# Optimization experiments

Measured on AMD Instinct MI355X. Metric: run time of the kernel, lower is better.

## Reference

```python
import jax, jax.numpy as jnp
import numpy as np

T, B, D_IN, H = 512, 128, 1024, 2048

def _lstm_cell(x, h, c, W_ih, W_hh, b):
    # PyTorch LSTMCell gate order: i, f, g, o
    gates = x @ W_ih.T + h @ W_hh.T + b  # [B, 4H]
    i, f, g, o = jnp.split(gates, 4, axis=-1)
    c_new = jax.nn.sigmoid(f) * c + jax.nn.sigmoid(i) * jnp.tanh(g)
    h_new = jax.nn.sigmoid(o) * jnp.tanh(c_new)
    return h_new, c_new

def setup_inputs() -> dict:
    key = jax.random.key(0)
    ks = jax.random.split(key, 12)
    k = 1.0 / np.sqrt(H)  # torch LSTMCell init range
    u = lambda kk, shape: jax.random.uniform(kk, shape, jnp.float32, -k, k)
    return {
        "input_seq": jax.random.normal(ks[0], (T, B, D_IN), jnp.float32),
        "h0": jax.random.normal(ks[1], (2, B, H), jnp.float32),
        "c0": jax.random.normal(ks[2], (2, B, H), jnp.float32),
        "W_ih0": u(ks[3], (4 * H, D_IN)),
        "W_hh0": u(ks[4], (4 * H, H)),
        "b0": u(ks[5], (4 * H,)),
        "W_ih1": u(ks[6], (4 * H, H)),
        "W_hh1": u(ks[7], (4 * H, H)),
        "b1": u(ks[8], (4 * H,)),
    }

def reference(input_seq, h0, c0, W_ih0, W_hh0, b0, W_ih1, W_hh1, b1):
    def step(carry, x_t):
        h0_, c0_, h1_, c1_ = carry
        h0n, c0n = _lstm_cell(x_t, h0_, c0_, W_ih0, W_hh0, b0)
        h1n, c1n = _lstm_cell(h0n, h1_, c1_, W_ih1, W_hh1, b1)
        return (h0n, c0n, h1n, c1n), None

    init = (h0[0], c0[0], h0[1], c0[1])
    (h0f, c0f, h1f, c1f), _ = jax.lax.scan(step, init, input_seq)
    return h1f  # last layer hidden at final timestep [B, H]
```

## Files before the change

### kernel.cpp

```cpp
#include <hip/hip_runtime.h>
#include <stdint.h>
#include <stddef.h>

#define T_STEPS 512
#define B_SZ    128
#define DIN     1024
#define H_SZ    2048
#define NG      8192
#define BH      (B_SZ * H_SZ)

typedef __attribute__((ext_vector_type(8))) short bf16x8;
typedef __attribute__((ext_vector_type(16))) float f32x16;

static __device__ __forceinline__ unsigned short f2bf(float x) {
  unsigned int u = __float_as_uint(x);
  u += 0x7fffu + ((u >> 16) & 1u);
  return (unsigned short)(u >> 16);
}

static __device__ __forceinline__ float sigm(float x) {
  return 1.0f / (1.0f + __expf(-x));
}
static __device__ __forceinline__ float tanh_(float x) {
  float e = __expf(-2.0f * fabsf(x));
  float t = (1.0f - e) / (1.0f + e);
  return x < 0.0f ? -t : t;
}

static __device__ __forceinline__ void async_load16(const void* gsrc, void* ldst) {
  __builtin_amdgcn_global_load_lds(
      (__attribute__((address_space(1))) void*)(const_cast<void*>(gsrc)),
      (__attribute__((address_space(3))) void*)ldst,
      16, 0, 0);
}

static __device__ __forceinline__ void wg_barrier_pinned() {
  __builtin_amdgcn_s_barrier();
  asm volatile("" ::: "memory");
  __builtin_amdgcn_sched_barrier(0);
}

static __device__ __forceinline__ void publish(unsigned* flag, unsigned epoch) {
  __syncthreads();
  if (threadIdx.x == 0) {
    __threadfence();
    __hip_atomic_store(flag, epoch, __ATOMIC_RELEASE, __HIP_MEMORY_SCOPE_AGENT);
  }
}
static __device__ __forceinline__ void await(const unsigned* flag, unsigned epoch) {
  if (threadIdx.x == 0)
    while (__hip_atomic_load(flag, __ATOMIC_ACQUIRE, __HIP_MEMORY_SCOPE_AGENT) < epoch)
      __builtin_amdgcn_s_sleep(8);
  __syncthreads();
}

__global__ void cvt_x_bf16(const float4* __restrict__ in, ushort4* __restrict__ out, int n4) {
  int i = blockIdx.x * blockDim.x + threadIdx.x;
  int st = gridDim.x * blockDim.x;
  for (; i < n4; i += st) {
    float4 v = in[i];
    ushort4 o;
    o.x = f2bf(v.x); o.y = f2bf(v.y); o.z = f2bf(v.z); o.w = f2bf(v.w);
    out[i] = o;
  }
}

__global__ void build_wcat(const float* __restrict__ wa, const float* __restrict__ wb,
                           unsigned short* __restrict__ outw, int ka, int K) {
  int k = blockIdx.x * blockDim.x + threadIdx.x;
  int n = blockIdx.y;
  if (k >= K) return;
  int kb = K - ka;
  float v = (k < ka) ? wa[(size_t)n * ka + k]
                     : wb[(size_t)n * kb + (k - ka)];
  outw[(size_t)n * K + k] = f2bf(v);
}

__global__ void init_state(const float* __restrict__ h0, const float* __restrict__ c0,
                           unsigned short* __restrict__ hb0, unsigned short* __restrict__ hb1,
                           float* __restrict__ cws, unsigned* __restrict__ flags) {
  int i = blockIdx.x * blockDim.x + threadIdx.x;
  if (i < 256) flags[i] = 0u;
  if (i < BH) {
    hb0[i] = f2bf(h0[i]);
    hb1[i] = f2bf(h0[BH + i]);
    cws[i] = c0[i];
    cws[BH + i] = c0[BH + i];
  }
}

template<int KT>
static __device__ __forceinline__ void gemm_ks(
    unsigned short (*Bbuf)[128 * 64],
    const unsigned short* __restrict__ a0, int s0, int ksplit,
    const unsigned short* __restrict__ a1,
    int kofs,
    const unsigned short* __restrict__ w, int wstr,
    int tid, int lane, int wv, int n0h,
    f32x16 (&acc)[4])
{
  const int arow = wv * 32 + (lane & 31);
  const unsigned short* r0p = a0 + (size_t)arow * s0;
  const unsigned short* r1p = a1 + (size_t)arow * H_SZ;
  const int khi = (lane >> 5) << 3;

  auto loadA = [&](int kt, bf16x8 (&A)[4]) {
    const int kbg = kofs + (kt << 6);
    const bool sA = kbg < ksplit;
    const unsigned short* bp = (sA ? r0p + kbg : r1p + (kbg - ksplit)) + khi;
#pragma unroll
    for (int cc = 0; cc < 4; ++cc)
      A[cc] = *(const bf16x8*)(bp + cc * 16);
  };

  auto stageB = [&](int kt) {
    const int kbg = kofs + (kt << 6);
#pragma unroll
    for (int it = 0; it < 4; ++it) {
      int cid = it * 256 + tid;
      int nl  = cid >> 3;
      int chs = (cid & 7) ^ (nl & 7);
      int nn  = ((nl >> 5) << 11) + n0h + (nl & 31);
      const unsigned short* src = w + (size_t)nn * wstr + kbg + (chs << 3);
      async_load16(src, &Bbuf[kt & 3][(it * 256 + wv * 64) * 8]);
    }
  };

  auto iter = [&](int kt, bf16x8 (&A)[4]) {
    if (kt + 3 < KT) stageB(kt + 3);
    const int bq = kt & 3;
#pragma unroll
    for (int cc = 0; cc < 4; ++cc) {
      const int chunk = (((cc << 1) + (lane >> 5)) ^ (lane & 7)) << 3;
      bf16x8 bfr[4];
#pragma unroll
      for (int ct = 0; ct < 4; ++ct)
        bfr[ct] = *(const bf16x8*)&Bbuf[bq][(ct * 32 + (lane & 31)) * 64 + chunk];
#pragma unroll
      for (int ct = 0; ct < 4; ++ct)
        acc[ct] = __builtin_amdgcn_mfma_f32_32x32x16_bf16(A[cc], bfr[ct], acc[ct], 0, 0, 0);
    }
    if (kt + 4 < KT) loadA(kt + 4, A);
    int rem = KT - 1 - kt;
    if (rem >= 4)      asm volatile("s_waitcnt vmcnt(20)" ::: "memory");
    else if (rem == 3) asm volatile("s_waitcnt vmcnt(16)" ::: "memory");
    else if (rem == 2) asm volatile("s_waitcnt vmcnt(8)"  ::: "memory");
    else if (rem == 1) asm volatile("s_waitcnt vmcnt(0)"  ::: "memory");
    if (rem > 0) wg_barrier_pinned();
  };

  asm volatile("s_waitcnt vmcnt(0)" ::: "memory");

  bf16x8 A0[4], A1[4], A2[4], A3[4];
  stageB(0); loadA(0, A0);
  stageB(1); loadA(1, A1);
  stageB(2); loadA(2, A2);
  loadA(3, A3);
  asm volatile("s_waitcnt vmcnt(24)" ::: "memory");
  wg_barrier_pinned();

  for (int kt = 0; kt < KT; kt += 4) {
    iter(kt,     A0);
    iter(kt + 1, A1);
    iter(kt + 2, A2);
    iter(kt + 3, A3);
  }
}

static __device__ __forceinline__ void store_partial(
    const f32x16 (&acc)[4], float* __restrict__ p, int lane, int wv) {
  const int col = lane & 31;
  const int rbase = wv * 32 + ((lane >> 5) << 2);
#pragma unroll
  for (int ct = 0; ct < 4; ++ct)
#pragma unroll
    for (int reg = 0; reg < 16; ++reg) {
      int row = rbase + (reg & 3) + ((reg >> 2) << 3);
      p[((ct << 7) + row) * 32 + col] = acc[ct][reg];
    }
}
static __device__ __forceinline__ void combine_add(
    f32x16 (&acc)[4], const float* __restrict__ p, int lane, int wv) {
  const int col = lane & 31;
  const int rbase = wv * 32 + ((lane >> 5) << 2);
#pragma unroll
  for (int ct = 0; ct < 4; ++ct)
#pragma unroll
    for (int reg = 0; reg < 16; ++reg) {
      int row = rbase + (reg & 3) + ((reg >> 2) << 3);
      acc[ct][reg] += p[((ct << 7) + row) * 32 + col];
    }
}

static __device__ __forceinline__ void lstm_epilogue(
    const f32x16 (&acc)[4], const float* __restrict__ bias,
    float* __restrict__ c, unsigned short* __restrict__ hout,
    float* __restrict__ fout, int lane, int wv, int n0h) {
  const int hc = n0h + (lane & 31);
  const float bi  = bias[hc];
  const float bff = bias[H_SZ + hc];
  const float bg  = bias[2 * H_SZ + hc];
  const float bo  = bias[3 * H_SZ + hc];
  const int rbase = wv * 32 + ((lane >> 5) << 2);
#pragma unroll
  for (int reg = 0; reg < 16; ++reg) {
    int row = rbase + (reg & 3) + ((reg >> 2) << 3);
    size_t idx = (size_t)row * H_SZ + hc;
    float iv = sigm(acc[0][reg] + bi);
    float fv = sigm(acc[1][reg] + bff);
    float gv = tanh_(acc[2][reg] + bg);
    float ov = sigm(acc[3][reg] + bo);
    float cn = fv * c[idx] + iv * gv;
    c[idx] = cn;
    float hn = ov * tanh_(cn);
    hout[idx] = f2bf(hn);
    if (fout) fout[idx] = hn;
  }
}

template<int KT1, int KT0>
__global__ __launch_bounds__(256) void lstm_pair_ks(
    const unsigned short* __restrict__ h0cur,
    const unsigned short* __restrict__ h1prev,
    const unsigned short* __restrict__ Wc1, const float* __restrict__ b1,
    float* __restrict__ c1, unsigned short* __restrict__ h1out,
    const unsigned short* __restrict__ xsl,
    const unsigned short* __restrict__ Wc0, const float* __restrict__ b0,
    float* __restrict__ c0, unsigned short* __restrict__ h0out,
    float* __restrict__ p1, float* __restrict__ p0,
    unsigned* __restrict__ f1, unsigned* __restrict__ f0, unsigned epoch)
{
  __shared__ __align__(16) unsigned short Bbuf[4][128 * 64];
  const int tid = threadIdx.x, lane = tid & 63, wv = tid >> 6;
  const int role = blockIdx.x >> 6, cb = blockIdx.x & 63, n0h = cb << 5;
  f32x16 acc[4] = {};

  if (role == 0) {
    gemm_ks<KT1>(Bbuf, h0cur, H_SZ, 2048, h1prev, 0, Wc1, 4096, tid, lane, wv, n0h, acc);
    await(f1 + cb, epoch);
    combine_add(acc, p1 + (size_t)cb * 16384, lane, wv);
    lstm_epilogue(acc, b1, c1, h1out, nullptr, lane, wv, n0h);
  } else if (role == 1) {
    gemm_ks<KT1>(Bbuf, h0cur, H_SZ, 2048, h1prev, 2048, Wc1, 4096, tid, lane, wv, n0h, acc);
    store_partial(acc, p1 + (size_t)cb * 16384, lane, wv);
    publish(f1 + cb, epoch);
  } else if (role == 2) {
    gemm_ks<KT0>(Bbuf, xsl, DIN, 1024, h0cur, 0, Wc0, 3072, tid, lane, wv, n0h, acc);
    await(f0 + cb, epoch);
    combine_add(acc, p0 + (size_t)cb * 16384, lane, wv);
    lstm_epilogue(acc, b0, c0, h0out, nullptr, lane, wv, n0h);
  } else {
    gemm_ks<KT0>(Bbuf, xsl, DIN, 1024, h0cur, 1536, Wc0, 3072, tid, lane, wv, n0h, acc);
    store_partial(acc, p0 + (size_t)cb * 16384, lane, wv);
    publish(f0 + cb, epoch);
  }
}

template<int KT>
__global__ __launch_bounds__(256) void lstm_solo_ks(
    const unsigned short* __restrict__ a0, int s0, int ksplit,
    const unsigned short* __restrict__ a1,
    int kofs1,
    const unsigned short* __restrict__ w, int wstr, const float* __restrict__ bias,
    float* __restrict__ c, unsigned short* __restrict__ hout, float* __restrict__ fout,
    float* __restrict__ part, unsigned* __restrict__ flg, unsigned epoch)
{
  __shared__ __align__(16) unsigned short Bbuf[4][128 * 64];
  const int tid = threadIdx.x, lane = tid & 63, wv = tid >> 6;
  const int half = blockIdx.x >> 6, cb = blockIdx.x & 63, n0h = cb << 5;
  f32x16 acc[4] = {};

  if (half == 0) {
    gemm_ks<KT>(Bbuf, a0, s0, ksplit, a1, 0, w, wstr, tid, lane, wv, n0h, acc);
    await(flg + cb, epoch);
    combine_add(acc, part + (size_t)cb * 16384, lane, wv);
    lstm_epilogue(acc, bias, c, hout, fout, lane, wv, n0h);
  } else {
    gemm_ks<KT>(Bbuf, a0, s0, ksplit, a1, kofs1, w, wstr, tid, lane, wv, n0h, acc);
    store_partial(acc, part + (size_t)cb * 16384, lane, wv);
    publish(flg + cb, epoch);
  }
}

extern "C" void kernel_launch(void* const* d_in, const int* in_sizes, int n_in,
                              void* d_out, int out_size, void* d_ws, size_t ws_size,
                              hipStream_t stream) {
  (void)in_sizes; (void)n_in; (void)out_size; (void)ws_size;
  const float* x    = (const float*)d_in[0];
  const float* h0   = (const float*)d_in[1];
  const float* c0   = (const float*)d_in[2];
  const float* Wih0 = (const float*)d_in[3];
  const float* Whh0 = (const float*)d_in[4];
  const float* b0   = (const float*)d_in[5];
  const float* Wih1 = (const float*)d_in[6];
  const float* Whh1 = (const float*)d_in[7];
  const float* b1   = (const float*)d_in[8];
  float* out = (float*)d_out;

  unsigned short* xbf = (unsigned short*)d_ws;
  unsigned short* Wc0 = xbf + (size_t)T_STEPS * B_SZ * DIN;
  unsigned short* Wc1 = Wc0 + (size_t)NG * 3072;
  unsigned short* hb0 = Wc1 + (size_t)NG * 4096;
  unsigned short* hb1 = hb0 + 2 * (size_t)BH;
  float*          cws = (float*)(hb1 + 2 * (size_t)BH);
  float*          p1  = cws + 2 * (size_t)BH;
  float*          p0  = p1 + 64 * 16384;
  unsigned*       flg = (unsigned*)(p0 + 64 * 16384);
  unsigned* flags1 = flg;
  unsigned* flags0 = flg + 64;
  unsigned* flagsE = flg + 128;

  cvt_x_bf16<<<dim3(4096), dim3(256), 0, stream>>>(
      (const float4*)x, (ushort4*)xbf, T_STEPS * B_SZ * DIN / 4);
  build_wcat<<<dim3(12, NG), dim3(256), 0, stream>>>(Wih0, Whh0, Wc0, DIN, 3072);
  build_wcat<<<dim3(16, NG), dim3(256), 0, stream>>>(Wih1, Whh1, Wc1, H_SZ, 4096);
  init_state<<<dim3(BH / 256), dim3(256), 0, stream>>>(h0, c0, hb0, hb1, cws, flg);

  lstm_solo_ks<24><<<dim3(128), dim3(256), 0, stream>>>(
      xbf, DIN, 1024, hb0 + 0, 1536, Wc0, 3072, b0,
      cws, hb0 + BH, nullptr, p0, flagsE, 1u);

  for (int t = 0; t < T_STEPS - 1; ++t) {
    const unsigned short* h0cur = hb0 + (size_t)((t + 1) & 1) * BH;
    lstm_pair_ks<32, 24><<<dim3(256), dim3(256), 0, stream>>>(
        h0cur, hb1 + (size_t)(t & 1) * BH, Wc1, b1,
        cws + BH, hb1 + (size_t)((t + 1) & 1) * BH,
        xbf + (size_t)(t + 1) * B_SZ * DIN, Wc0, b0,
        cws, hb0 + (size_t)(t & 1) * BH,
        p1, p0, flags1, flags0, (unsigned)(t + 1));
  }
  lstm_solo_ks<32><<<dim3(128), dim3(256), 0, stream>>>(
      hb0 + 0, H_SZ, 2048, hb1 + BH, 2048, Wc1, 4096, b1,
      cws + BH, hb1 + 0, out, p1, flagsE + 64, 1u);
}
```

Baseline: 21.68 ms.

## Fuse 16 LSTM timesteps per launch with grid-wide counter synchronization

Replaces one kernel launch per timestep with a persistent-style kernel that loops over up to 16 timesteps. Cross-block dependencies between timesteps are enforced through global atomic counters (h0/h1 produced counts and read-done counts for double-buffer reuse). The aim is to remove per-step launch overhead and the implicit grid barrier between steps. In exchange it relies on all 256 blocks being co-resident and on correct counter protocols, which risks deadlock or races if occupancy assumptions fail.

Measured after the change: 70.23 ms. 3.24x slower.

```diff
diff --git a/kernel.cpp b/kernel.cpp
--- a/kernel.cpp
+++ b/kernel.cpp
@@ -52,6 +52,24 @@
     while (__hip_atomic_load(flag, __ATOMIC_ACQUIRE, __HIP_MEMORY_SCOPE_AGENT) < epoch)
       __builtin_amdgcn_s_sleep(8);
   __syncthreads();
+}
+static __device__ __forceinline__ void await_ge(const unsigned* p, unsigned tgt) {
+  if (threadIdx.x == 0)
+    while (__hip_atomic_load(p, __ATOMIC_ACQUIRE, __HIP_MEMORY_SCOPE_AGENT) < tgt)
+      __builtin_amdgcn_s_sleep(32);
+  __syncthreads();
+}
+static __device__ __forceinline__ void post_cnt(unsigned* p) {
+  __syncthreads();
+  if (threadIdx.x == 0)
+    __hip_atomic_fetch_add(p, 1u, __ATOMIC_RELEASE, __HIP_MEMORY_SCOPE_AGENT);
+}
+static __device__ __forceinline__ void post_data(unsigned* p) {
+  __syncthreads();
+  if (threadIdx.x == 0) {
+    __threadfence();
+    __hip_atomic_fetch_add(p, 1u, __ATOMIC_RELEASE, __HIP_MEMORY_SCOPE_AGENT);
+  }
 }
 
 __global__ void cvt_x_bf16(const float4* __restrict__ in, ushort4* __restrict__ out, int n4) {
@@ -80,7 +98,7 @@
                            unsigned short* __restrict__ hb0, unsigned short* __restrict__ hb1,
                            float* __restrict__ cws, unsigned* __restrict__ flags) {
   int i = blockIdx.x * blockDim.x + threadIdx.x;
-  if (i < 256) flags[i] = 0u;
+  if (i < 262) flags[i] = (i == 256 || i == 257) ? 64u : 0u;
   if (i < BH) {
     hb0[i] = f2bf(h0[i]);
     hb1[i] = f2bf(h0[BH + i]);
@@ -219,40 +237,68 @@
 }
 
 template<int KT1, int KT0>
-__global__ __launch_bounds__(256) void lstm_pair_ks(
-    const unsigned short* __restrict__ h0cur,
-    const unsigned short* __restrict__ h1prev,
+__global__ __launch_bounds__(256) void lstm_fused(
+    const unsigned short* __restrict__ xbf,
     const unsigned short* __restrict__ Wc1, const float* __restrict__ b1,
-    float* __restrict__ c1, unsigned short* __restrict__ h1out,
-    const unsigned short* __restrict__ xsl,
     const unsigned short* __restrict__ Wc0, const float* __restrict__ b0,
-    float* __restrict__ c0, unsigned short* __restrict__ h0out,
+    unsigned short* __restrict__ hb0, unsigned short* __restrict__ hb1,
+    float* __restrict__ c1buf, float* __restrict__ c0buf,
     float* __restrict__ p1, float* __restrict__ p0,
-    unsigned* __restrict__ f1, unsigned* __restrict__ f0, unsigned epoch)
+    unsigned* __restrict__ flg, int tbase, int G)
 {
   __shared__ __align__(16) unsigned short Bbuf[4][128 * 64];
   const int tid = threadIdx.x, lane = tid & 63, wv = tid >> 6;
   const int role = blockIdx.x >> 6, cb = blockIdx.x & 63, n0h = cb << 5;
-  f32x16 acc[4] = {};
-
-  if (role == 0) {
-    gemm_ks<KT1>(Bbuf, h0cur, H_SZ, 2048, h1prev, 0, Wc1, 4096, tid, lane, wv, n0h, acc);
-    await(f1 + cb, epoch);
-    combine_add(acc, p1 + (size_t)cb * 16384, lane, wv);
-    lstm_epilogue(acc, b1, c1, h1out, nullptr, lane, wv, n0h);
-  } else if (role == 1) {
-    gemm_ks<KT1>(Bbuf, h0cur, H_SZ, 2048, h1prev, 2048, Wc1, 4096, tid, lane, wv, n0h, acc);
-    store_partial(acc, p1 + (size_t)cb * 16384, lane, wv);
-    publish(f1 + cb, epoch);
-  } else if (role == 2) {
-    gemm_ks<KT0>(Bbuf, xsl, DIN, 1024, h0cur, 0, Wc0, 3072, tid, lane, wv, n0h, acc);
-    await(f0 + cb, epoch);
-    combine_add(acc, p0 + (size_t)cb * 16384, lane, wv);
-    lstm_epilogue(acc, b0, c0, h0out, nullptr, lane, wv, n0h);
-  } else {
-    gemm_ks<KT0>(Bbuf, xsl, DIN, 1024, h0cur, 1536, Wc0, 3072, tid, lane, wv, n0h, acc);
-    store_partial(acc, p0 + (size_t)cb * 16384, lane, wv);
-    publish(f0 + cb, epoch);
+  unsigned* f1    = flg;
+  unsigned* f0    = flg + 64;
+  unsigned* h0cnt = flg + 256;
+  unsigned* h1cnt = flg + 257;
+  unsigned* h0rd2 = flg + 258;
+  unsigned* h1rd2 = flg + 260;
+
+  for (int g = 0; g < G; ++g) {
+    const int t = tbase + g;
+    const unsigned short* h0cur = hb0 + (size_t)((t + 1) & 1) * BH;
+    const unsigned prior = (unsigned)((t + 1) >> 1);
+    f32x16 acc[4] = {};
+
+    if (role == 0) {
+      await_ge(h0cnt, 64u * (t + 1));
+      gemm_ks<KT1>(Bbuf, h0cur, H_SZ, 2048, hb1 + (size_t)(t & 1) * BH, 0,
+                   Wc1, 4096, tid, lane, wv, n0h, acc);
+      post_cnt(h0rd2 + ((t + 1) & 1));
+      await(f1 + cb, (unsigned)(t + 1));
+      combine_add(acc, p1 + (size_t)cb * 16384, lane, wv);
+      await_ge(h1rd2 + ((t + 1) & 1), 64u * prior);
+      lstm_epilogue(acc, b1, c1buf, hb1 + (size_t)((t + 1) & 1) * BH,
+                    nullptr, lane, wv, n0h);
+      post_data(h1cnt);
+    } else if (role == 1) {
+      await_ge(h1cnt, 64u * (t + 1));
+      gemm_ks<KT1>(Bbuf, h0cur, H_SZ, 2048, hb1 + (size_t)(t & 1) * BH, 2048,
+                   Wc1, 4096, tid, lane, wv, n0h, acc);
+      post_cnt(h1rd2 + (t & 1));
+      store_partial(acc, p1 + (size_t)cb * 16384, lane, wv);
+      publish(f1 + cb, (unsigned)(t + 1));
+    } else if (role == 2) {
+      await_ge(h0cnt, 64u * (t + 1));
+      gemm_ks<KT0>(Bbuf, xbf + (size_t)(t + 1) * B_SZ * DIN, DIN, 1024, h0cur, 0,
+                   Wc0, 3072, tid, lane, wv, n0h, acc);
+      post_cnt(h0rd2 + ((t + 1) & 1));
+      await(f0 + cb, (unsigned)(t + 1));
+      combine_add(acc, p0 + (size_t)cb * 16384, lane, wv);
+      await_ge(h0rd2 + (t & 1), 192u * prior);
+      lstm_epilogue(acc, b0, c0buf, hb0 + (size_t)(t & 1) * BH,
+                    nullptr, lane, wv, n0h);
+      post_data(h0cnt);
+    } else {
+      await_ge(h0cnt, 64u * (t + 1));
+      gemm_ks<KT0>(Bbuf, xbf + (size_t)(t + 1) * B_SZ * DIN, DIN, 1024, h0cur, 1536,
+                   Wc0, 3072, tid, lane, wv, n0h, acc);
+      post_cnt(h0rd2 + ((t + 1) & 1));
+      store_partial(acc, p0 + (size_t)cb * 16384, lane, wv);
+      publish(f0 + cb, (unsigned)(t + 1));
+    }
   }
 }
 
@@ -306,8 +352,6 @@
   float*          p1  = cws + 2 * (size_t)BH;
   float*          p0  = p1 + 64 * 16384;
   unsigned*       flg = (unsigned*)(p0 + 64 * 16384);
-  unsigned* flags1 = flg;
-  unsigned* flags0 = flg + 64;
   unsigned* flagsE = flg + 128;
 
   cvt_x_bf16<<<dim3(4096), dim3(256), 0, stream>>>(
@@ -320,15 +364,15 @@
       xbf, DIN, 1024, hb0 + 0, 1536, Wc0, 3072, b0,
       cws, hb0 + BH, nullptr, p0, flagsE, 1u);
 
-  for (int t = 0; t < T_STEPS - 1; ++t) {
-    const unsigned short* h0cur = hb0 + (size_t)((t + 1) & 1) * BH;
-    lstm_pair_ks<32, 24><<<dim3(256), dim3(256), 0, stream>>>(
-        h0cur, hb1 + (size_t)(t & 1) * BH, Wc1, b1,
-        cws + BH, hb1 + (size_t)((t + 1) & 1) * BH,
-        xbf + (size_t)(t + 1) * B_SZ * DIN, Wc0, b0,
-        cws, hb0 + (size_t)(t & 1) * BH,
-        p1, p0, flags1, flags0, (unsigned)(t + 1));
-  }
+  int t = 0;
+  while (t < T_STEPS - 1) {
+    int G = (T_STEPS - 1 - t < 16) ? (T_STEPS - 1 - t) : 16;
+    lstm_fused<32, 24><<<dim3(256), dim3(256), 0, stream>>>(
+        xbf, Wc1, b1, Wc0, b0, hb0, hb1,
+        cws + BH, cws, p1, p0, flg, t, G);
+    t += G;
+  }
+
   lstm_solo_ks<32><<<dim3(128), dim3(256), 0, stream>>>(
       hb0 + 0, H_SZ, 2048, hb1 + BH, 2048, Wc1, 4096, b1,
       cws + BH, hb1 + 0, out, p1, flagsE + 64, 1u);
```
